# Performance work log

Hardware: AMD Instinct MI355X
Metric: run time of the kernel (lower is better)

Reference implementation:

```python
import jax, jax.numpy as jnp
import numpy as np

N, IN_DIM, OUT_DIM, H = 4096, 128, 128, 4
HEAD_DIM = OUT_DIM // H
NEG_SLOPE = 0.2


def setup_inputs() -> dict:
    key = jax.random.key(0)
    k1, k2, k3, k4, k5 = jax.random.split(key, 5)
    x = jax.random.normal(k1, (N, IN_DIM), dtype=jnp.float32)
    adj = jax.random.randint(k2, (N, N), 0, 2, dtype=jnp.int32)
    # nn.Linear(in_dim, out_dim, bias=False): weight is [out_dim, in_dim]
    W = jax.random.normal(k3, (OUT_DIM, IN_DIM), dtype=jnp.float32) * (1.0 / np.sqrt(IN_DIM))
    attn_src = jax.random.normal(k4, (1, H, HEAD_DIM), dtype=jnp.float32) * 0.1
    attn_dst = jax.random.normal(k5, (1, H, HEAD_DIM), dtype=jnp.float32) * 0.1
    return {"x": x, "adj": adj, "W": W, "attn_src": attn_src, "attn_dst": attn_dst}


def reference(x, adj, W, attn_src, attn_dst):
    n = x.shape[0]
    h = (x @ W.T).reshape(n, H, HEAD_DIM)            # [N, H, D]
    e_src = jnp.sum(h * attn_src, axis=-1)           # [N, H]
    e_dst = jnp.sum(h * attn_dst, axis=-1)           # [N, H]
    e = e_src[:, None, :] + e_dst[None, :, :]        # [N, N, H]
    e = jax.nn.leaky_relu(e, negative_slope=NEG_SLOPE)
    e = jnp.where((adj == 0)[:, :, None], -jnp.inf, e)
    alpha = jax.nn.softmax(e, axis=1)                # softmax over neighbors j
    # dropout omitted (eval mode)
    out = jnp.einsum('ijh,jhd->ihd', alpha, h)       # [N, H, D]
    return out.reshape(n, -1)
```

## Files before the change

### kernel.cpp

```cpp
#include <hip/hip_runtime.h>
#include <hip/hip_bf16.h>

#define NN 4096
#define SJ 8
#define JCH (NN / SJ)
#define JSTEP 64
#define NSTEPS (JCH / JSTEP)
#define LOG2E 1.44269504f

typedef __attribute__((ext_vector_type(4))) float f32x4;
typedef __attribute__((ext_vector_type(4))) int i32x4;
typedef __attribute__((ext_vector_type(4))) unsigned int u32x4;
typedef __attribute__((ext_vector_type(8))) short short8;

__device__ __forceinline__ unsigned pk2(float a, float b) {
    float2 t; t.x = a; t.y = b;
    __hip_bfloat162 h = __float22bfloat162_rn(t);
    unsigned r;
    __builtin_memcpy(&r, &h, 4);
    return r;
}

__device__ __forceinline__ short8 load8_bf(const float* __restrict__ p) {
    f32x4 a = *(const f32x4*)p;
    f32x4 b = *(const f32x4*)(p + 4);
    u32x4 v = {pk2(a[0], a[1]), pk2(a[2], a[3]), pk2(b[0], b[1]), pk2(b[2], b[3])};
    return __builtin_bit_cast(short8, v);
}

__global__ __launch_bounds__(256) void k1_proj(
        const float* __restrict__ x, const float* __restrict__ W,
        const float* __restrict__ asrc, const float* __restrict__ adst,
        unsigned short* __restrict__ hT, float* __restrict__ Rt,
        unsigned* __restrict__ BDt) {
    __shared__ unsigned short ttile[4][32][16];
    const int ibase = blockIdx.x * 16;
    const int w = threadIdx.x >> 6;
    const int lane = threadIdx.x & 63;
    const int grp = lane >> 4, li = lane & 15;

    const float* xrow = x + (ibase + li) * 128;
    const float* w0 = W + (w * 32 + li) * 128;
    const float* w1 = W + (w * 32 + 16 + li) * 128;

    f32x4 c0 = {0.f, 0.f, 0.f, 0.f}, c1 = {0.f, 0.f, 0.f, 0.f};
#pragma unroll
    for (int ko = 0; ko < 128; ko += 32) {
        const int kk = ko + grp * 8;
        short8 a = load8_bf(xrow + kk);
        short8 b0 = load8_bf(w0 + kk);
        short8 b1 = load8_bf(w1 + kk);
        c0 = __builtin_amdgcn_mfma_f32_16x16x32_bf16(a, b0, c0, 0, 0, 0);
        c1 = __builtin_amdgcn_mfma_f32_16x16x32_bf16(a, b1, c1, 0, 0, 0);
    }
    const float as0 = asrc[w * 32 + li], as1 = asrc[w * 32 + 16 + li];
    const float ad0 = adst[w * 32 + li], ad1 = adst[w * 32 + 16 + li];
    float pes[4], ped[4];
#pragma unroll
    for (int r = 0; r < 4; ++r) {
        pes[r] = c0[r] * as0 + c1[r] * as1;
        ped[r] = c0[r] * ad0 + c1[r] * ad1;
    }
#pragma unroll
    for (int m = 1; m < 16; m <<= 1) {
#pragma unroll
        for (int r = 0; r < 4; ++r) {
            pes[r] += __shfl_xor(pes[r], m);
            ped[r] += __shfl_xor(ped[r], m);
        }
    }
    if (li == 0) {
#pragma unroll
        for (int r = 0; r < 4; ++r) {
            const int row = ibase + grp * 4 + r;
            Rt[w * NN + row] = __builtin_amdgcn_exp2f(-0.8f * LOG2E * pes[r]);
            const float Bv = __builtin_amdgcn_exp2f(LOG2E * ped[r]);
            const float Dv = __builtin_amdgcn_exp2f(0.2f * LOG2E * ped[r]);
            BDt[w * NN + row] = pk2(Bv, Dv);
        }
    }
    unsigned short* tw = &ttile[w][0][0];
    {
        uint2 v0; v0.x = pk2(c0[0], c0[1]); v0.y = pk2(c0[2], c0[3]);
        uint2 v1; v1.x = pk2(c1[0], c1[1]); v1.y = pk2(c1[2], c1[3]);
        *(uint2*)&tw[li * 16 + grp * 4] = v0;
        *(uint2*)&tw[(li + 16) * 16 + grp * 4] = v1;
    }
    __syncthreads();
    const int d = lane >> 1, half = lane & 1;
    u32x4 v = *(const u32x4*)&ttile[w][d][half * 8];
    *(u32x4*)(hT + (size_t)(w * 32 + d) * NN + ibase + half * 8) = v;
}

__device__ __forceinline__ u32x4 gld0(const void* p) {
    u32x4 d; asm volatile("global_load_dwordx4 %0, %1, off" : "=&v"(d) : "v"(p)); return d;
}
__device__ __forceinline__ u32x4 gld16(const void* p) {
    u32x4 d; asm volatile("global_load_dwordx4 %0, %1, off offset:16" : "=&v"(d) : "v"(p)); return d;
}
__device__ __forceinline__ u32x4 gld64(const void* p) {
    u32x4 d; asm volatile("global_load_dwordx4 %0, %1, off offset:64" : "=&v"(d) : "v"(p)); return d;
}
__device__ __forceinline__ u32x4 gld128(const void* p) {
    u32x4 d; asm volatile("global_load_dwordx4 %0, %1, off offset:128" : "=&v"(d) : "v"(p)); return d;
}
__device__ __forceinline__ u32x4 gld144(const void* p) {
    u32x4 d; asm volatile("global_load_dwordx4 %0, %1, off offset:144" : "=&v"(d) : "v"(p)); return d;
}

struct SR { u32x4 h0k0, h0k1, h1k0, h1k1, bd00, bd01, bd10, bd11; };

#define LOADR(dst, toff) do {                                             \
    (dst).h0k0 = gld0(h0b + (toff));  (dst).h0k1 = gld64(h0b + (toff));   \
    (dst).h1k0 = gld0(h1b + (toff));  (dst).h1k1 = gld64(h1b + (toff));   \
    (dst).bd00 = gld0(bd + (toff));   (dst).bd01 = gld16(bd + (toff));    \
    (dst).bd10 = gld128(bd + (toff)); (dst).bd11 = gld144(bd + (toff));   \
} while (0)

#define LAUNDER(s) asm volatile("" : "+v"((s).h0k0), "+v"((s).h0k1),      \
    "+v"((s).h1k0), "+v"((s).h1k1), "+v"((s).bd00), "+v"((s).bd01),       \
    "+v"((s).bd10), "+v"((s).bd11))

__device__ __forceinline__ short8 buildQ(float R, const u32x4 ba, const u32x4 bb,
                                         const i32x4 q0, const i32x4 q1) {
    float p[8];
#pragma unroll
    for (int e = 0; e < 4; ++e) {
        const unsigned v = ba[e];
        const float B = __builtin_bit_cast(float, v << 16);
        const float D = __builtin_bit_cast(float, v & 0xFFFF0000u);
        const float m = fmaxf(B, R * D);
        p[e] = __builtin_bit_cast(float, __builtin_bit_cast(unsigned, m) & (0u - (unsigned)q0[e]));
    }
#pragma unroll
    for (int e = 0; e < 4; ++e) {
        const unsigned v = bb[e];
        const float B = __builtin_bit_cast(float, v << 16);
        const float D = __builtin_bit_cast(float, v & 0xFFFF0000u);
        const float m = fmaxf(B, R * D);
        p[4 + e] = __builtin_bit_cast(float, __builtin_bit_cast(unsigned, m) & (0u - (unsigned)q1[e]));
    }
    u32x4 u = {pk2(p[0], p[1]), pk2(p[2], p[3]), pk2(p[4], p[5]), pk2(p[6], p[7])};
    return __builtin_bit_cast(short8, u);
}

__global__ __launch_bounds__(256) void k3_main(
        const int* __restrict__ adj, const unsigned short* __restrict__ hT,
        const float* __restrict__ Rt, const unsigned* __restrict__ BDt,
        float* __restrict__ numer, float* __restrict__ denom) {
    __shared__ unsigned int adjbuf[3][32 * 64];

    const int ibase = blockIdx.x * 32;
    const int jstart = blockIdx.y * JCH;
    const int head = threadIdx.x >> 6;
    const int lane = threadIdx.x & 63;
    const int grp = lane >> 4, li = lane & 15;

    const float R0 = Rt[head * NN + ibase + li];
    const float R1 = Rt[head * NN + ibase + 16 + li];
    const unsigned short* h0b = hT + (size_t)(head * 32 + li) * NN + jstart + grp * 8;
    const unsigned short* h1b = h0b + (size_t)16 * NN;
    const unsigned* bd = BDt + head * NN + jstart + grp * 8;
    const unsigned int* adju = (const unsigned int*)adj;

    const int Rw0 = head * 8 + grp, Rw1 = Rw0 + 4;
    const unsigned int* g0 = adju + (size_t)(ibase + Rw0) * NN + jstart + (li ^ (Rw0 & 15)) * 4;
    const unsigned int* g1 = adju + (size_t)(ibase + Rw1) * NN + jstart + (li ^ (Rw1 & 15)) * 4;

    f32x4 c00 = {0.f,0.f,0.f,0.f}, c01 = {0.f,0.f,0.f,0.f};
    f32x4 c10 = {0.f,0.f,0.f,0.f}, c11 = {0.f,0.f,0.f,0.f};
    f32x4 dn0 = {0.f,0.f,0.f,0.f}, dn1 = {0.f,0.f,0.f,0.f};
    short8 bones;
#pragma unroll
    for (int e = 0; e < 8; ++e) bones[e] = (short)0x3F80;

    auto stage = [&](int slot, int s) {
        __builtin_amdgcn_global_load_lds(g0 + s * JSTEP, &adjbuf[slot][(head * 8) * 64], 16, 0, 0);
        __builtin_amdgcn_global_load_lds(g1 + s * JSTEP, &adjbuf[slot][(head * 8 + 4) * 64], 16, 0, 0);
    };
    auto compute = [&](const unsigned int* buf, const SR& S) {
#pragma unroll
        for (int ks = 0; ks < 2; ++ks) {
            const u32x4 ba = ks ? S.bd10 : S.bd00;
            const u32x4 bb = ks ? S.bd11 : S.bd01;
            const short8 tA = __builtin_bit_cast(short8, ks ? S.h0k1 : S.h0k0);
            const short8 tB = __builtin_bit_cast(short8, ks ? S.h1k1 : S.h1k0);
            const int cb = ks * 8 + grp * 2;
            const i32x4 q00 = *(const i32x4*)&buf[li * 64 + ((cb) ^ li) * 4];
            const i32x4 q01 = *(const i32x4*)&buf[li * 64 + ((cb + 1) ^ li) * 4];
            const i32x4 q10 = *(const i32x4*)&buf[(li + 16) * 64 + ((cb) ^ li) * 4];
            const i32x4 q11 = *(const i32x4*)&buf[(li + 16) * 64 + ((cb + 1) ^ li) * 4];
            const short8 A0 = buildQ(R0, ba, bb, q00, q01);
            const short8 A1 = buildQ(R1, ba, bb, q10, q11);
            c00 = __builtin_amdgcn_mfma_f32_16x16x32_bf16(A0, tA, c00, 0, 0, 0);
            c01 = __builtin_amdgcn_mfma_f32_16x16x32_bf16(A0, tB, c01, 0, 0, 0);
            c10 = __builtin_amdgcn_mfma_f32_16x16x32_bf16(A1, tA, c10, 0, 0, 0);
            c11 = __builtin_amdgcn_mfma_f32_16x16x32_bf16(A1, tB, c11, 0, 0, 0);
            dn0 = __builtin_amdgcn_mfma_f32_16x16x32_bf16(A0, bones, dn0, 0, 0, 0);
            dn1 = __builtin_amdgcn_mfma_f32_16x16x32_bf16(A1, bones, dn1, 0, 0, 0);
        }
    };

    SR S0, S1;
    stage(0, 0);
    __builtin_amdgcn_sched_barrier(0);
    LOADR(S0, 0);
    __builtin_amdgcn_sched_barrier(0);
    stage(1, 1);
    __builtin_amdgcn_sched_barrier(0);
    asm volatile("s_waitcnt vmcnt(2)" ::: "memory");
    LAUNDER(S0);
    __builtin_amdgcn_s_barrier();
    __builtin_amdgcn_sched_barrier(0);

#pragma unroll
    for (int t = 0; t < NSTEPS; ++t) {
        SR& Scur = (t & 1) ? S1 : S0;
        SR& Snxt = (t & 1) ? S0 : S1;
        if (t + 1 < NSTEPS) { LOADR(Snxt, (t + 1) * JSTEP); }
        __builtin_amdgcn_sched_barrier(0);
        if (t + 2 < NSTEPS) stage((t + 2) % 3, t + 2);
        __builtin_amdgcn_sched_barrier(0);

        compute(&adjbuf[t % 3][0], Scur);

        if (t + 1 < NSTEPS) {
            if (t + 2 < NSTEPS) {
                asm volatile("s_waitcnt vmcnt(2)" ::: "memory");
            } else {
                asm volatile("s_waitcnt vmcnt(0)" ::: "memory");
            }
            LAUNDER(Snxt);
            __builtin_amdgcn_s_barrier();
            __builtin_amdgcn_sched_barrier(0);
        }
    }

    const int r0 = ibase + grp * 4;
    float* nb = numer + head * 32 + li;
#pragma unroll
    for (int r = 0; r < 4; ++r) {
        atomicAdd(nb + (size_t)(r0 + r) * 128, c00[r]);
        atomicAdd(nb + (size_t)(r0 + r) * 128 + 16, c01[r]);
        atomicAdd(nb + (size_t)(r0 + 16 + r) * 128, c10[r]);
        atomicAdd(nb + (size_t)(r0 + 16 + r) * 128 + 16, c11[r]);
    }
    if (li == 0) {
#pragma unroll
        for (int r = 0; r < 4; ++r) {
            atomicAdd(denom + (r0 + r) * 4 + head, dn0[r]);
            atomicAdd(denom + (r0 + 16 + r) * 4 + head, dn1[r]);
        }
    }
}

__global__ __launch_bounds__(256) void k4_fin(const float* __restrict__ numer,
                                              const float* __restrict__ denom,
                                              float* __restrict__ out) {
    const int idx = blockIdx.x * 256 + threadIdx.x;
    const int node = idx >> 7;
    const int headc = (idx & 127) >> 5;
    out[idx] = numer[idx] / denom[node * 4 + headc];
}

extern "C" void kernel_launch(void* const* d_in, const int* in_sizes, int n_in,
                              void* d_out, int out_size, void* d_ws, size_t ws_size,
                              hipStream_t stream) {
    const float* x = (const float*)d_in[0];
    const int* adj = (const int*)d_in[1];
    const float* W = (const float*)d_in[2];
    const float* asrc = (const float*)d_in[3];
    const float* adst = (const float*)d_in[4];
    float* out = (float*)d_out;

    char* ws = (char*)d_ws;
    float* numer = (float*)ws;
    float* denom = (float*)(ws + (size_t)2097152);
    float* Rt = (float*)(ws + (size_t)2097152 + 65536);
    unsigned* BDt = (unsigned*)(ws + (size_t)2097152 + 131072);
    unsigned short* hT = (unsigned short*)(ws + (size_t)2097152 + 196608);

    (void)hipMemsetAsync(numer, 0, 2097152 + 65536, stream);
    k1_proj<<<256, 256, 0, stream>>>(x, W, asrc, adst, hT, Rt, BDt);
    k3_main<<<dim3(128, SJ), 256, 0, stream>>>(adj, hT, Rt, BDt, numer, denom);
    k4_fin<<<2048, 256, 0, stream>>>(numer, denom, out);
}
```

Before: 57.45 us.

## Stage BD coefficients through LDS and deepen hT register prefetch to three buffers

The per-column B/D coefficients move from per-lane register loads (four 16-byte loads per step) into a shared triple-buffered LDS slot filled with global_load_lds, so each step now issues one small load per lane instead of four. The hT operand prefetch goes from double to triple buffering in registers, issued two steps ahead, with the vmcnt waits adjusted to match. The intent is fewer redundant global loads and more latency hiding, in exchange for more VGPR pressure from the third register set and extra LDS reads in the inner loop.

```diff
diff --git a/kernel.cpp b/kernel.cpp
--- a/kernel.cpp
+++ b/kernel.cpp
@@ -95,31 +95,19 @@
 __device__ __forceinline__ u32x4 gld0(const void* p) {
     u32x4 d; asm volatile("global_load_dwordx4 %0, %1, off" : "=&v"(d) : "v"(p)); return d;
 }
-__device__ __forceinline__ u32x4 gld16(const void* p) {
-    u32x4 d; asm volatile("global_load_dwordx4 %0, %1, off offset:16" : "=&v"(d) : "v"(p)); return d;
-}
 __device__ __forceinline__ u32x4 gld64(const void* p) {
     u32x4 d; asm volatile("global_load_dwordx4 %0, %1, off offset:64" : "=&v"(d) : "v"(p)); return d;
 }
-__device__ __forceinline__ u32x4 gld128(const void* p) {
-    u32x4 d; asm volatile("global_load_dwordx4 %0, %1, off offset:128" : "=&v"(d) : "v"(p)); return d;
-}
-__device__ __forceinline__ u32x4 gld144(const void* p) {
-    u32x4 d; asm volatile("global_load_dwordx4 %0, %1, off offset:144" : "=&v"(d) : "v"(p)); return d;
-}
-
-struct SR { u32x4 h0k0, h0k1, h1k0, h1k1, bd00, bd01, bd10, bd11; };
-
-#define LOADR(dst, toff) do {                                             \
+
+struct HT { u32x4 h0k0, h0k1, h1k0, h1k1; };
+
+#define LOADHT(dst, toff) do {                                            \
     (dst).h0k0 = gld0(h0b + (toff));  (dst).h0k1 = gld64(h0b + (toff));   \
     (dst).h1k0 = gld0(h1b + (toff));  (dst).h1k1 = gld64(h1b + (toff));   \
-    (dst).bd00 = gld0(bd + (toff));   (dst).bd01 = gld16(bd + (toff));    \
-    (dst).bd10 = gld128(bd + (toff)); (dst).bd11 = gld144(bd + (toff));   \
 } while (0)
 
-#define LAUNDER(s) asm volatile("" : "+v"((s).h0k0), "+v"((s).h0k1),      \
-    "+v"((s).h1k0), "+v"((s).h1k1), "+v"((s).bd00), "+v"((s).bd01),       \
-    "+v"((s).bd10), "+v"((s).bd11))
+#define LAUNDHT(s) asm volatile("" : "+v"((s).h0k0), "+v"((s).h0k1),      \
+    "+v"((s).h1k0), "+v"((s).h1k1))
 
 __device__ __forceinline__ short8 buildQ(float R, const u32x4 ba, const u32x4 bb,
                                          const i32x4 q0, const i32x4 q1) {
@@ -148,7 +136,8 @@
         const int* __restrict__ adj, const unsigned short* __restrict__ hT,
         const float* __restrict__ Rt, const unsigned* __restrict__ BDt,
         float* __restrict__ numer, float* __restrict__ denom) {
-    __shared__ unsigned int adjbuf[3][32 * 64];
+    __shared__ unsigned int adjb[3][32 * 64];
+    __shared__ unsigned int bdb[3][4 * 64];
 
     const int ibase = blockIdx.x * 32;
     const int jstart = blockIdx.y * JCH;
@@ -160,7 +149,7 @@
     const float R1 = Rt[head * NN + ibase + 16 + li];
     const unsigned short* h0b = hT + (size_t)(head * 32 + li) * NN + jstart + grp * 8;
     const unsigned short* h1b = h0b + (size_t)16 * NN;
-    const unsigned* bd = BDt + head * NN + jstart + grp * 8;
+    const unsigned* bdsrc = BDt + head * NN + jstart + lane;
     const unsigned int* adju = (const unsigned int*)adj;
 
     const int Rw0 = head * 8 + grp, Rw1 = Rw0 + 4;
@@ -174,22 +163,25 @@
 #pragma unroll
     for (int e = 0; e < 8; ++e) bones[e] = (short)0x3F80;
 
+    HT ht0, ht1, ht2;
+
     auto stage = [&](int slot, int s) {
-        __builtin_amdgcn_global_load_lds(g0 + s * JSTEP, &adjbuf[slot][(head * 8) * 64], 16, 0, 0);
-        __builtin_amdgcn_global_load_lds(g1 + s * JSTEP, &adjbuf[slot][(head * 8 + 4) * 64], 16, 0, 0);
+        __builtin_amdgcn_global_load_lds(g0 + s * JSTEP, &adjb[slot][(head * 8) * 64], 16, 0, 0);
+        __builtin_amdgcn_global_load_lds(g1 + s * JSTEP, &adjb[slot][(head * 8 + 4) * 64], 16, 0, 0);
+        __builtin_amdgcn_global_load_lds(bdsrc + s * JSTEP, &bdb[slot][head * 64], 4, 0, 0);
     };
-    auto compute = [&](const unsigned int* buf, const SR& S) {
+    auto compute = [&](const unsigned int* abuf, const unsigned int* bbuf, const HT& S) {
 #pragma unroll
         for (int ks = 0; ks < 2; ++ks) {
-            const u32x4 ba = ks ? S.bd10 : S.bd00;
-            const u32x4 bb = ks ? S.bd11 : S.bd01;
+            const u32x4 ba = *(const u32x4*)&bbuf[head * 64 + ks * 32 + grp * 8];
+            const u32x4 bb = *(const u32x4*)&bbuf[head * 64 + ks * 32 + grp * 8 + 4];
             const short8 tA = __builtin_bit_cast(short8, ks ? S.h0k1 : S.h0k0);
             const short8 tB = __builtin_bit_cast(short8, ks ? S.h1k1 : S.h1k0);
             const int cb = ks * 8 + grp * 2;
-            const i32x4 q00 = *(const i32x4*)&buf[li * 64 + ((cb) ^ li) * 4];
-            const i32x4 q01 = *(const i32x4*)&buf[li * 64 + ((cb + 1) ^ li) * 4];
-            const i32x4 q10 = *(const i32x4*)&buf[(li + 16) * 64 + ((cb) ^ li) * 4];
-            const i32x4 q11 = *(const i32x4*)&buf[(li + 16) * 64 + ((cb + 1) ^ li) * 4];
+            const i32x4 q00 = *(const i32x4*)&abuf[li * 64 + ((cb) ^ li) * 4];
+            const i32x4 q01 = *(const i32x4*)&abuf[li * 64 + ((cb + 1) ^ li) * 4];
+            const i32x4 q10 = *(const i32x4*)&abuf[(li + 16) * 64 + ((cb) ^ li) * 4];
+            const i32x4 q11 = *(const i32x4*)&abuf[(li + 16) * 64 + ((cb + 1) ^ li) * 4];
             const short8 A0 = buildQ(R0, ba, bb, q00, q01);
             const short8 A1 = buildQ(R1, ba, bb, q10, q11);
             c00 = __builtin_amdgcn_mfma_f32_16x16x32_bf16(A0, tA, c00, 0, 0, 0);
@@ -201,36 +193,41 @@
         }
     };
 
-    SR S0, S1;
+    LOADHT(ht0, 0);
+    __builtin_amdgcn_sched_barrier(0);
     stage(0, 0);
     __builtin_amdgcn_sched_barrier(0);
-    LOADR(S0, 0);
+    LOADHT(ht1, JSTEP);
     __builtin_amdgcn_sched_barrier(0);
     stage(1, 1);
     __builtin_amdgcn_sched_barrier(0);
-    asm volatile("s_waitcnt vmcnt(2)" ::: "memory");
-    LAUNDER(S0);
+    asm volatile("s_waitcnt vmcnt(7)" ::: "memory");
+    LAUNDHT(ht0);
     __builtin_amdgcn_s_barrier();
     __builtin_amdgcn_sched_barrier(0);
 
 #pragma unroll
     for (int t = 0; t < NSTEPS; ++t) {
-        SR& Scur = (t & 1) ? S1 : S0;
-        SR& Snxt = (t & 1) ? S0 : S1;
-        if (t + 1 < NSTEPS) { LOADR(Snxt, (t + 1) * JSTEP); }
-        __builtin_amdgcn_sched_barrier(0);
-        if (t + 2 < NSTEPS) stage((t + 2) % 3, t + 2);
-        __builtin_amdgcn_sched_barrier(0);
-
-        compute(&adjbuf[t % 3][0], Scur);
+        HT& Scur = (t % 3 == 0) ? ht0 : ((t % 3 == 1) ? ht1 : ht2);
+        HT& Snxt = ((t + 1) % 3 == 0) ? ht0 : (((t + 1) % 3 == 1) ? ht1 : ht2);
+        HT& Sfar = ((t + 2) % 3 == 0) ? ht0 : (((t + 2) % 3 == 1) ? ht1 : ht2);
+
+        if (t + 2 < NSTEPS) {
+            LOADHT(Sfar, (t + 2) * JSTEP);
+            __builtin_amdgcn_sched_barrier(0);
+            stage((t + 2) % 3, t + 2);
+            __builtin_amdgcn_sched_barrier(0);
+        }
+
+        compute(&adjb[t % 3][0], &bdb[t % 3][0], Scur);
 
         if (t + 1 < NSTEPS) {
             if (t + 2 < NSTEPS) {
-                asm volatile("s_waitcnt vmcnt(2)" ::: "memory");
+                asm volatile("s_waitcnt vmcnt(7)" ::: "memory");
             } else {
                 asm volatile("s_waitcnt vmcnt(0)" ::: "memory");
             }
-            LAUNDER(Snxt);
+            LAUNDHT(Snxt);
             __builtin_amdgcn_s_barrier();
             __builtin_amdgcn_sched_barrier(0);
         }
```

Result: slower. 59.30 us (+3.2%).

## Give each head wave private adjacency buffers and drop block barriers

Applied to the files above, without the earlier changes.

Halves the row tile to 16 nodes per block and gives each wave its own triple-buffered LDS copy of the adjacency tile, so waves no longer synchronise with block-wide barriers. The grid is doubled to keep coverage. The cost is that each head wave now loads the full adjacency tile itself, quadrupling adjacency load requests. It also doubles LDS use per block and reloads the h/BD operands for half as many rows.

```diff
diff --git a/kernel.cpp b/kernel.cpp
--- a/kernel.cpp
+++ b/kernel.cpp
@@ -148,35 +148,38 @@
         const int* __restrict__ adj, const unsigned short* __restrict__ hT,
         const float* __restrict__ Rt, const unsigned* __restrict__ BDt,
         float* __restrict__ numer, float* __restrict__ denom) {
-    __shared__ unsigned int adjbuf[3][32 * 64];
-
-    const int ibase = blockIdx.x * 32;
+    __shared__ unsigned int adjb[4][3][16 * 64];
+
+    const int ibase = blockIdx.x * 16;
     const int jstart = blockIdx.y * JCH;
     const int head = threadIdx.x >> 6;
     const int lane = threadIdx.x & 63;
     const int grp = lane >> 4, li = lane & 15;
+    const int sub = lane >> 4, p = lane & 15;
 
     const float R0 = Rt[head * NN + ibase + li];
-    const float R1 = Rt[head * NN + ibase + 16 + li];
     const unsigned short* h0b = hT + (size_t)(head * 32 + li) * NN + jstart + grp * 8;
     const unsigned short* h1b = h0b + (size_t)16 * NN;
     const unsigned* bd = BDt + head * NN + jstart + grp * 8;
     const unsigned int* adju = (const unsigned int*)adj;
 
-    const int Rw0 = head * 8 + grp, Rw1 = Rw0 + 4;
-    const unsigned int* g0 = adju + (size_t)(ibase + Rw0) * NN + jstart + (li ^ (Rw0 & 15)) * 4;
-    const unsigned int* g1 = adju + (size_t)(ibase + Rw1) * NN + jstart + (li ^ (Rw1 & 15)) * 4;
-
-    f32x4 c00 = {0.f,0.f,0.f,0.f}, c01 = {0.f,0.f,0.f,0.f};
-    f32x4 c10 = {0.f,0.f,0.f,0.f}, c11 = {0.f,0.f,0.f,0.f};
-    f32x4 dn0 = {0.f,0.f,0.f,0.f}, dn1 = {0.f,0.f,0.f,0.f};
+    const unsigned int* g[4];
+#pragma unroll
+    for (int k = 0; k < 4; ++k) {
+        const int r = k * 4 + sub;
+        g[k] = adju + (size_t)(ibase + r) * NN + jstart + (p ^ (r & 15)) * 4;
+    }
+
+    f32x4 c0 = {0.f,0.f,0.f,0.f}, c1 = {0.f,0.f,0.f,0.f}, dn = {0.f,0.f,0.f,0.f};
     short8 bones;
 #pragma unroll
     for (int e = 0; e < 8; ++e) bones[e] = (short)0x3F80;
 
     auto stage = [&](int slot, int s) {
-        __builtin_amdgcn_global_load_lds(g0 + s * JSTEP, &adjbuf[slot][(head * 8) * 64], 16, 0, 0);
-        __builtin_amdgcn_global_load_lds(g1 + s * JSTEP, &adjbuf[slot][(head * 8 + 4) * 64], 16, 0, 0);
+#pragma unroll
+        for (int k = 0; k < 4; ++k)
+            __builtin_amdgcn_global_load_lds(g[k] + s * JSTEP,
+                                             &adjb[head][slot][k * 4 * 64], 16, 0, 0);
     };
     auto compute = [&](const unsigned int* buf, const SR& S) {
 #pragma unroll
@@ -186,31 +189,24 @@
             const short8 tA = __builtin_bit_cast(short8, ks ? S.h0k1 : S.h0k0);
             const short8 tB = __builtin_bit_cast(short8, ks ? S.h1k1 : S.h1k0);
             const int cb = ks * 8 + grp * 2;
-            const i32x4 q00 = *(const i32x4*)&buf[li * 64 + ((cb) ^ li) * 4];
-            const i32x4 q01 = *(const i32x4*)&buf[li * 64 + ((cb + 1) ^ li) * 4];
-            const i32x4 q10 = *(const i32x4*)&buf[(li + 16) * 64 + ((cb) ^ li) * 4];
-            const i32x4 q11 = *(const i32x4*)&buf[(li + 16) * 64 + ((cb + 1) ^ li) * 4];
-            const short8 A0 = buildQ(R0, ba, bb, q00, q01);
-            const short8 A1 = buildQ(R1, ba, bb, q10, q11);
-            c00 = __builtin_amdgcn_mfma_f32_16x16x32_bf16(A0, tA, c00, 0, 0, 0);
-            c01 = __builtin_amdgcn_mfma_f32_16x16x32_bf16(A0, tB, c01, 0, 0, 0);
-            c10 = __builtin_amdgcn_mfma_f32_16x16x32_bf16(A1, tA, c10, 0, 0, 0);
-            c11 = __builtin_amdgcn_mfma_f32_16x16x32_bf16(A1, tB, c11, 0, 0, 0);
-            dn0 = __builtin_amdgcn_mfma_f32_16x16x32_bf16(A0, bones, dn0, 0, 0, 0);
-            dn1 = __builtin_amdgcn_mfma_f32_16x16x32_bf16(A1, bones, dn1, 0, 0, 0);
+            const i32x4 q0 = *(const i32x4*)&buf[li * 64 + ((cb) ^ li) * 4];
+            const i32x4 q1 = *(const i32x4*)&buf[li * 64 + ((cb + 1) ^ li) * 4];
+            const short8 A = buildQ(R0, ba, bb, q0, q1);
+            c0 = __builtin_amdgcn_mfma_f32_16x16x32_bf16(A, tA, c0, 0, 0, 0);
+            c1 = __builtin_amdgcn_mfma_f32_16x16x32_bf16(A, tB, c1, 0, 0, 0);
+            dn = __builtin_amdgcn_mfma_f32_16x16x32_bf16(A, bones, dn, 0, 0, 0);
         }
     };
 
     SR S0, S1;
+    LOADR(S0, 0);
+    __builtin_amdgcn_sched_barrier(0);
     stage(0, 0);
     __builtin_amdgcn_sched_barrier(0);
-    LOADR(S0, 0);
-    __builtin_amdgcn_sched_barrier(0);
     stage(1, 1);
     __builtin_amdgcn_sched_barrier(0);
-    asm volatile("s_waitcnt vmcnt(2)" ::: "memory");
+    asm volatile("s_waitcnt vmcnt(4)" ::: "memory");
     LAUNDER(S0);
-    __builtin_amdgcn_s_barrier();
     __builtin_amdgcn_sched_barrier(0);
 
 #pragma unroll
@@ -222,16 +218,15 @@
         if (t + 2 < NSTEPS) stage((t + 2) % 3, t + 2);
         __builtin_amdgcn_sched_barrier(0);
 
-        compute(&adjbuf[t % 3][0], Scur);
+        compute(&adjb[head][t % 3][0], Scur);
 
         if (t + 1 < NSTEPS) {
             if (t + 2 < NSTEPS) {
-                asm volatile("s_waitcnt vmcnt(2)" ::: "memory");
+                asm volatile("s_waitcnt vmcnt(4)" ::: "memory");
             } else {
                 asm volatile("s_waitcnt vmcnt(0)" ::: "memory");
             }
             LAUNDER(Snxt);
-            __builtin_amdgcn_s_barrier();
             __builtin_amdgcn_sched_barrier(0);
         }
     }
@@ -240,17 +235,13 @@
     float* nb = numer + head * 32 + li;
 #pragma unroll
     for (int r = 0; r < 4; ++r) {
-        atomicAdd(nb + (size_t)(r0 + r) * 128, c00[r]);
-        atomicAdd(nb + (size_t)(r0 + r) * 128 + 16, c01[r]);
-        atomicAdd(nb + (size_t)(r0 + 16 + r) * 128, c10[r]);
-        atomicAdd(nb + (size_t)(r0 + 16 + r) * 128 + 16, c11[r]);
+        atomicAdd(nb + (size_t)(r0 + r) * 128, c0[r]);
+        atomicAdd(nb + (size_t)(r0 + r) * 128 + 16, c1[r]);
     }
     if (li == 0) {
 #pragma unroll
-        for (int r = 0; r < 4; ++r) {
-            atomicAdd(denom + (r0 + r) * 4 + head, dn0[r]);
-            atomicAdd(denom + (r0 + 16 + r) * 4 + head, dn1[r]);
-        }
+        for (int r = 0; r < 4; ++r)
+            atomicAdd(denom + (r0 + r) * 4 + head, dn[r]);
     }
 }
 
@@ -282,6 +273,6 @@
 
     (void)hipMemsetAsync(numer, 0, 2097152 + 65536, stream);
     k1_proj<<<256, 256, 0, stream>>>(x, W, asrc, adst, hT, Rt, BDt);
-    k3_main<<<dim3(128, SJ), 256, 0, stream>>>(adj, hT, Rt, BDt, numer, denom);
+    k3_main<<<dim3(256, SJ), 256, 0, stream>>>(adj, hT, Rt, BDt, numer, denom);
     k4_fin<<<2048, 256, 0, stream>>>(numer, denom, out);
 }
```

After: 70.38 us. 22.5% more time.
